# Kernel tuning notes

Measured on AMD Instinct MI355X. Metric: run time of the kernel, lower is better.

The kernel has to match this reference:

```python
import jax, jax.numpy as jnp
import numpy as np

N = 100000      # nodes
M_HE = 200000   # hyperedges
E = 2000000     # incidences (edge_index columns)
IN, HID, OUT, NT = 16, 64, 64, 2


def setup_inputs() -> dict:
    key = jax.random.key(0)
    ks = jax.random.split(key, 16)
    s = 0.05
    return {
        "x": jax.random.normal(ks[0], (N, IN), jnp.float32),
        "h_prev": jax.random.normal(ks[1], (N, HID), jnp.float32),
        "edge_nodes": jax.random.randint(ks[2], (E,), 0, N, dtype=jnp.int32),
        "edge_hedges": jax.random.randint(ks[3], (E,), 0, M_HE, dtype=jnp.int32),
        "edge_attr": jax.random.randint(ks[4], (E,), 0, NT, dtype=jnp.int32),
        "W_conv": jax.random.normal(ks[5], (NT, IN, HID), jnp.float32) * s,
        "b_conv": jax.random.normal(ks[6], (NT, HID), jnp.float32) * s,
        "W_mix": jax.random.normal(ks[7], (NT * HID, HID), jnp.float32) * s,
        "b_mix": jax.random.normal(ks[8], (HID,), jnp.float32) * s,
        "W_ih": jax.random.normal(ks[9], (3 * HID, HID), jnp.float32) * s,
        "W_hh": jax.random.normal(ks[10], (3 * HID, HID), jnp.float32) * s,
        "b_ih": jax.random.normal(ks[11], (3 * HID,), jnp.float32) * s,
        "b_hh": jax.random.normal(ks[12], (3 * HID,), jnp.float32) * s,
        "W_out": jax.random.normal(ks[13], (HID, OUT), jnp.float32) * s,
        "b_out": jax.random.normal(ks[14], (OUT,), jnp.float32) * s,
    }


def _hconv(x, W, b, nodes, hedges, mask_f):
    """PyG HypergraphConv: out = D^-1 H B^-1 H^T (x W) + b, restricted to
    incidences where mask_f==1 (replaces torch nonzero()-based slicing)."""
    xw = x @ W                                                   # [N, HID]
    Bdeg = jax.ops.segment_sum(mask_f, hedges, num_segments=M_HE)  # |e| per hyperedge
    Ddeg = jax.ops.segment_sum(mask_f, nodes, num_segments=N)      # deg per node
    Binv = jnp.where(Bdeg > 0, 1.0 / Bdeg, 0.0)
    Dinv = jnp.where(Ddeg > 0, 1.0 / Ddeg, 0.0)
    # node -> hyperedge gather/scatter
    e_feat = jax.ops.segment_sum(xw[nodes] * mask_f[:, None], hedges,
                                 num_segments=M_HE) * Binv[:, None]  # [M_HE, HID]
    # hyperedge -> node gather/scatter
    out = jax.ops.segment_sum(e_feat[hedges] * mask_f[:, None], nodes,
                              num_segments=N) * Dinv[:, None]        # [N, HID]
    return out + b


def reference(x, h_prev, edge_nodes, edge_hedges, edge_attr,
              W_conv, b_conv, W_mix, b_mix,
              W_ih, W_hh, b_ih, b_hh, W_out, b_out):
    outs = []
    for t in range(NT):  # fixed small loop over edge types
        mask_f = (edge_attr == t).astype(x.dtype)
        outs.append(_hconv(x, W_conv[t], b_conv[t], edge_nodes, edge_hedges, mask_f))
    h = jax.nn.relu(jnp.concatenate(outs, axis=1) @ W_mix + b_mix)  # [N, HID]
    # torch GRUCell(h, h_prev)
    gi = h @ W_ih.T + b_ih
    gh = h_prev @ W_hh.T + b_hh
    i_r, i_z, i_n = jnp.split(gi, 3, axis=1)
    h_r, h_z, h_n = jnp.split(gh, 3, axis=1)
    r = jax.nn.sigmoid(i_r + h_r)
    z = jax.nn.sigmoid(i_z + h_z)
    n = jnp.tanh(i_n + r * h_n)
    h_next = (1.0 - z) * n + z * h_prev
    pred_xyz = (h_next @ W_out + b_out)[:, :3]
    return h_next, pred_xyz
```

## Files before the change

kernel.cpp:

```cpp
#include <hip/hip_runtime.h>

#define NN      100000
#define MHE     200000
#define EE      2000000
#define H1      400000
#define K2N     200000
#define NB1     782
#define NB2     782
#define NCB2    320
#define CHK2    6250
#define FCN     500480
#define SCB2    489
#define CAP1    3584
#define CAP2    3584
#define NT      6250

typedef unsigned short u16;
typedef unsigned int   u32;
typedef unsigned long long ull;
typedef __attribute__((ext_vector_type(8))) short  s16x8;
typedef __attribute__((ext_vector_type(4))) float  f32x4;
typedef __attribute__((ext_vector_type(4))) unsigned int u32x4;

__device__ __forceinline__ float bf2f(u16 u) { return __uint_as_float(((u32)u) << 16); }
__device__ __forceinline__ u16 f2bf(float f) {
    u32 u = __float_as_uint(f);
    return (u16)((u + 0x7fffu + ((u >> 16) & 1u)) >> 16);
}
__device__ __forceinline__ float ldv(const void* p, long i, int isf32) {
    return isf32 ? ((const float*)p)[i] : bf2f(((const u16*)p)[i]);
}
__device__ __forceinline__ u16 ldb(const void* p, long i, int isf32) {
    return isf32 ? f2bf(((const float*)p)[i]) : ((const u16*)p)[i];
}
__device__ __forceinline__ void stv(void* p, long i, float v, int isf32) {
    if (isf32) ((float*)p)[i] = v;
    else       ((u16*)p)[i] = f2bf(v);
}

union FragU { s16x8 v; ull q[2]; u16 u[8]; };

__device__ __forceinline__ s16x8 ld8bf(const void* p, long off, int isf32) {
    FragU f;
    if (isf32) {
        const float* fp = (const float*)p + off;
        f32x4 a = *(const f32x4*)fp;
        f32x4 b = *(const f32x4*)(fp + 4);
        f.u[0]=f2bf(a[0]); f.u[1]=f2bf(a[1]); f.u[2]=f2bf(a[2]); f.u[3]=f2bf(a[3]);
        f.u[4]=f2bf(b[0]); f.u[5]=f2bf(b[1]); f.u[6]=f2bf(b[2]); f.u[7]=f2bf(b[3]);
    } else {
        u32x4 w = *(const u32x4*)((const u16*)p + off);
        f.q[0] = ((ull)w[1] << 32) | w[0];
        f.q[1] = ((ull)w[3] << 32) | w[2];
    }
    return f.v;
}

__device__ __forceinline__ float frcp_(float x) { return __builtin_amdgcn_rcpf(x); }
__device__ __forceinline__ float sigm(float x)  { return frcp_(1.f + __expf(-x)); }
__device__ __forceinline__ float tanhf_(float x){ return 1.f - 2.f * frcp_(1.f + __expf(2.f * x)); }

#define OFF_BKT1  0
#define OFF_BKT2  2000000
#define OFF_EXB   4000000
#define OFF_FSC   7200000
#define OFF_TOT   7700481
#define OFF_BCOMB 7700970
#define OFF_WIHB  7701034
#define OFF_WHHB  7707178
#define OFF_WCB   7713322
#define OFF_FLAG  7714346

__global__ void detect_kernel(const u32* __restrict__ xw, u32* __restrict__ flag) {
    __shared__ int cnt;
    if (threadIdx.x == 0) cnt = 0;
    __syncthreads();
    int hits = 0;
    for (int i = threadIdx.x; i < 1024; i += 256) {
        float v = bf2f((u16)(xw[i] & 0xffffu));
        if (!(fabsf(v) < 1e10f)) hits++;
    }
    atomicAdd(&cnt, hits);
    __syncthreads();
    if (threadIdx.x == 0) flag[0] = (cnt >= 16) ? 1u : 0u;
}

#define XBASE 26688
__global__ __launch_bounds__(256) void setup_kernel(
        const void* __restrict__ W_conv, const void* __restrict__ b_conv,
        const void* __restrict__ W_mix,  const void* __restrict__ b_mix,
        const void* __restrict__ W_ih,   const void* __restrict__ W_hh,
        float* __restrict__ bcomb, u16* __restrict__ Wihb, u16* __restrict__ Whhb,
        u16* __restrict__ Wcb, const u32* __restrict__ flag) {
    int isf = (int)flag[0];
    int gid = blockIdx.x * 256 + threadIdx.x;
    if (gid < 12288) {
        Wihb[gid] = ldb(W_ih, gid, isf);
    } else if (gid < 24576) {
        int i = gid - 12288;
        Whhb[i] = ldb(W_hh, i, isf);
    } else if (gid < 26624) {
        int i = gid - 24576;
        int j = i >> 5, k = i & 31;
        int t0 = k >> 4, kk = k & 15;
        float acc = 0.f;
        for (int c = 0; c < 64; c++)
            acc += ldv(W_conv, (t0 * 16 + kk) * 64 + c, isf) * ldv(W_mix, (t0 * 64 + c) * 64 + j, isf);
        Wcb[i] = f2bf(acc);
    } else if (gid < XBASE) {
        int j = gid - 26624;
        if (j < 64) {
            float acc = ldv(b_mix, j, isf);
            for (int c = 0; c < 128; c++)
                acc += ldv(b_conv, c, isf) * ldv(W_mix, c * 64 + j, isf);
            bcomb[j] = acc;
        }
    }
}

__global__ __launch_bounds__(1024) void countC(const int* __restrict__ en, const int* __restrict__ eh,
                                               const int* __restrict__ ea, int* __restrict__ fcnt) {
    __shared__ int c[NB1 + NB2];
    int g = blockIdx.x, tid = threadIdx.x;
    for (int i = tid; i < NB1 + NB2; i += 1024) c[i] = 0;
    __syncthreads();
    int s = g * CHK2;
    for (int i = s + tid; i < s + CHK2; i += 1024) {
        int t = ea[i];
        atomicAdd(&c[(t * MHE + eh[i]) >> 9], 1);
        atomicAdd(&c[NB1 + ((t * NN + en[i]) >> 8)], 1);
    }
    __syncthreads();
    for (int b = tid; b < NB1 + NB2; b += 1024) fcnt[b * NCB2 + g] = c[b];
}

__global__ __launch_bounds__(256) void scanA2(int* __restrict__ a, int* __restrict__ tot) {
    __shared__ int lds[256];
    int g = blockIdx.x, t = threadIdx.x;
    int base = g * 1024 + t * 4;
    int v[4]; int s = 0;
    #pragma unroll
    for (int j = 0; j < 4; j++) { v[j] = (base + j < FCN) ? a[base + j] : 0; s += v[j]; }
    lds[t] = s;
    __syncthreads();
    for (int d = 1; d < 256; d <<= 1) {
        int tmp = (t >= d) ? lds[t - d] : 0;
        __syncthreads();
        lds[t] += tmp;
        __syncthreads();
    }
    int run = lds[t] - s;
    #pragma unroll
    for (int j = 0; j < 4; j++) { if (base + j < FCN) a[base + j] = run; run += v[j]; }
    if (t == 255) tot[g] = lds[255];
}

__global__ __launch_bounds__(1024) void scanB2(int* __restrict__ tot) {
    __shared__ int lds[1024];
    int t = threadIdx.x;
    int v = (t < SCB2) ? tot[t] : 0;
    lds[t] = v;
    __syncthreads();
    for (int d = 1; d < 1024; d <<= 1) {
        int tmp = (t >= d) ? lds[t - d] : 0;
        __syncthreads();
        lds[t] += tmp;
        __syncthreads();
    }
    if (t < SCB2) tot[t] = lds[t] - v;
}

__global__ __launch_bounds__(256) void scanC2(int* __restrict__ a, const int* __restrict__ tot) {
    int g = blockIdx.x, t = threadIdx.x;
    int add = tot[g];
    int base = g * 1024 + t * 4;
    #pragma unroll
    for (int j = 0; j < 4; j++)
        if (base + j < FCN) a[base + j] += add;
    if (g == 0 && t == 0) a[FCN] = 2 * EE;
}

template<int SIDE>
__global__ __launch_bounds__(1024) void placeC(const int* __restrict__ en, const int* __restrict__ eh,
                                               const int* __restrict__ ea, const int* __restrict__ fscan,
                                               u32* __restrict__ bktout) {
    __shared__ u32 sarr[CHK2];
    __shared__ int sbuf[1024];
    __shared__ int cnt[NB1];
    __shared__ int loff[NB1];
    const int nb = SIDE ? NB2 : NB1;
    const int fbase = SIDE ? NB1 * NCB2 : 0;
    int g = blockIdx.x, tid = threadIdx.x;
    for (int b = tid; b < nb; b += 1024) {
        int idx = fbase + b * NCB2 + g;
        cnt[b] = fscan[idx + 1] - fscan[idx];
    }
    __syncthreads();
    int v = (tid < nb) ? cnt[tid] : 0;
    sbuf[tid] = v;
    __syncthreads();
    for (int d = 1; d < 1024; d <<= 1) {
        int tmp = (tid >= d) ? sbuf[tid - d] : 0;
        __syncthreads();
        sbuf[tid] += tmp;
        __syncthreads();
    }
    if (tid < nb) { loff[tid] = sbuf[tid] - v; cnt[tid] = 0; }
    __syncthreads();
    int s = g * CHK2;
    for (int i = s + tid; i < s + CHK2; i += 1024) {
        int t = ea[i]; int nd = en[i]; int hh = eh[i];
        int k = SIDE ? (t * NN + nd) : (t * MHE + hh);
        int b = SIDE ? (k >> 8) : (k >> 9);
        int r = atomicAdd(&cnt[b], 1);
        u32 pay = SIDE ? (((u32)(k & 255) << 19) | (u32)(t * MHE + hh))
                       : (((u32)(k & 511) << 17) | (u32)nd);
        sarr[loff[b] + r] = pay;
    }
    __syncthreads();
    for (int s2 = tid; s2 < CHK2; s2 += 1024) {
        int lo = 0, hi = nb - 1;
        while (lo < hi) {
            int mid = (lo + hi + 1) >> 1;
            if (loff[mid] <= s2) lo = mid; else hi = mid - 1;
        }
        int gp = fscan[fbase + lo * NCB2 + g] + (s2 - loff[lo]);
        if (SIDE) gp -= EE;
        bktout[gp] = sarr[s2];
    }
}

__global__ __launch_bounds__(512) void hopA(const int* __restrict__ fscan, const u32* __restrict__ bkt1,
                                            const void* __restrict__ x, u32* __restrict__ exb,
                                            const u32* __restrict__ flag) {
    __shared__ int fcnt[512], foff[513], sbuf[512];
    __shared__ int snod[CAP1];
    int isf = (int)flag[0];
    int c = blockIdx.x, tid = threadIdx.x;
    int beg = fscan[c * NCB2], end = fscan[(c + 1) * NCB2];
    fcnt[tid] = 0;
    __syncthreads();
    for (int i = beg + tid; i < end; i += 512)
        atomicAdd(&fcnt[bkt1[i] >> 17], 1);
    __syncthreads();
    int v = fcnt[tid];
    sbuf[tid] = v;
    __syncthreads();
    for (int d = 1; d < 512; d <<= 1) {
        int tmp = (tid >= d) ? sbuf[tid - d] : 0;
        __syncthreads();
        sbuf[tid] += tmp;
        __syncthreads();
    }
    foff[tid] = sbuf[tid] - v;
    fcnt[tid] = 0;
    if (tid == 511) foff[512] = sbuf[511];
    __syncthreads();
    for (int i = beg + tid; i < end; i += 512) {
        u32 p = bkt1[i];
        int k = (int)(p >> 17);
        int r = atomicAdd(&fcnt[k], 1);
        snod[foff[k] + r] = (int)(p & 0x1FFFFu);
    }
    __syncthreads();
    int sub = tid & 7, grp = tid >> 3;
    for (int kk = grp; kk < 512; kk += 64) {
        int key = c * 512 + kk;
        if (key >= H1) break;
        int fb = foff[kk], fe = foff[kk + 1];
        float a0 = 0.f, a1 = 0.f, b0 = 0.f, b1 = 0.f;
        float c0 = 0.f, c1 = 0.f, d0 = 0.f, d1 = 0.f;
        int j = fb;
        if (isf) {
            const float* xf = (const float*)x;
            for (; j + 3 < fe; j += 4) {
                long n0 = (long)snod[j], n1 = (long)snod[j+1];
                long n2 = (long)snod[j+2], n3 = (long)snod[j+3];
                a0 += xf[n0 * 16 + 2 * sub]; a1 += xf[n0 * 16 + 2 * sub + 1];
                b0 += xf[n1 * 16 + 2 * sub]; b1 += xf[n1 * 16 + 2 * sub + 1];
                c0 += xf[n2 * 16 + 2 * sub]; c1 += xf[n2 * 16 + 2 * sub + 1];
                d0 += xf[n3 * 16 + 2 * sub]; d1 += xf[n3 * 16 + 2 * sub + 1];
            }
            for (; j < fe; j++) {
                long n0 = (long)snod[j];
                a0 += xf[n0 * 16 + 2 * sub];
                a1 += xf[n0 * 16 + 2 * sub + 1];
            }
        } else {
            const u32* xu = (const u32*)x;
            for (; j + 3 < fe; j += 4) {
                u32 w0 = xu[(long)snod[j]   * 8 + sub];
                u32 w1 = xu[(long)snod[j+1] * 8 + sub];
                u32 w2 = xu[(long)snod[j+2] * 8 + sub];
                u32 w3 = xu[(long)snod[j+3] * 8 + sub];
                a0 += bf2f((u16)(w0 & 0xffffu)); a1 += bf2f((u16)(w0 >> 16));
                b0 += bf2f((u16)(w1 & 0xffffu)); b1 += bf2f((u16)(w1 >> 16));
                c0 += bf2f((u16)(w2 & 0xffffu)); c1 += bf2f((u16)(w2 >> 16));
                d0 += bf2f((u16)(w3 & 0xffffu)); d1 += bf2f((u16)(w3 >> 16));
            }
            for (; j < fe; j++) {
                u32 w = xu[(long)snod[j] * 8 + sub];
                a0 += bf2f((u16)(w & 0xffffu));
                a1 += bf2f((u16)(w >> 16));
            }
        }
        float s0 = (a0 + b0) + (c0 + d0);
        float s1 = (a1 + b1) + (c1 + d1);
        int d = fe - fb;
        float inv = d > 0 ? 1.0f / (float)d : 0.f;
        exb[(long)key * 8 + sub] = (u32)f2bf(s0 * inv) | ((u32)f2bf(s1 * inv) << 16);
    }
}

__global__ __launch_bounds__(256) void hopB(const int* __restrict__ fscan, const u32* __restrict__ bkt2,
                                            const u32* __restrict__ exb, u32* __restrict__ aggb) {
    __shared__ int fcnt[256], foff[257], sbuf[256];
    __shared__ int shed[CAP2];
    int c = blockIdx.x, tid = threadIdx.x;
    int beg = fscan[NB1 * NCB2 + c * NCB2] - EE;
    int end = fscan[NB1 * NCB2 + (c + 1) * NCB2] - EE;
    fcnt[tid] = 0;
    __syncthreads();
    for (int i = beg + tid; i < end; i += 256)
        atomicAdd(&fcnt[bkt2[i] >> 19], 1);
    __syncthreads();
    int v = fcnt[tid];
    sbuf[tid] = v;
    __syncthreads();
    for (int d = 1; d < 256; d <<= 1) {
        int tmp = (tid >= d) ? sbuf[tid - d] : 0;
        __syncthreads();
        sbuf[tid] += tmp;
        __syncthreads();
    }
    foff[tid] = sbuf[tid] - v;
    fcnt[tid] = 0;
    if (tid == 255) foff[256] = sbuf[255];
    __syncthreads();
    for (int i = beg + tid; i < end; i += 256) {
        u32 p = bkt2[i];
        int k = (int)(p >> 19);
        int r = atomicAdd(&fcnt[k], 1);
        shed[foff[k] + r] = (int)(p & 0x7FFFFu);
    }
    __syncthreads();
    int sub = tid & 7, grp = tid >> 3;
    for (int kk = grp; kk < 256; kk += 32) {
        int key = c * 256 + kk;
        if (key >= K2N) break;
        int fb = foff[kk], fe = foff[kk + 1];
        float a0 = 0.f, a1 = 0.f, b0 = 0.f, b1 = 0.f;
        float c0 = 0.f, c1 = 0.f, d0 = 0.f, d1 = 0.f;
        int j = fb;
        for (; j + 3 < fe; j += 4) {
            u32 w0 = exb[(long)shed[j]   * 8 + sub];
            u32 w1 = exb[(long)shed[j+1] * 8 + sub];
            u32 w2 = exb[(long)shed[j+2] * 8 + sub];
            u32 w3 = exb[(long)shed[j+3] * 8 + sub];
            a0 += bf2f((u16)(w0 & 0xffffu)); a1 += bf2f((u16)(w0 >> 16));
            b0 += bf2f((u16)(w1 & 0xffffu)); b1 += bf2f((u16)(w1 >> 16));
            c0 += bf2f((u16)(w2 & 0xffffu)); c1 += bf2f((u16)(w2 >> 16));
            d0 += bf2f((u16)(w3 & 0xffffu)); d1 += bf2f((u16)(w3 >> 16));
        }
        for (; j < fe; j++) {
            u32 w = exb[(long)shed[j] * 8 + sub];
            a0 += bf2f((u16)(w & 0xffffu));
            a1 += bf2f((u16)(w >> 16));
        }
        float s0 = (a0 + b0) + (c0 + d0);
        float s1 = (a1 + b1) + (c1 + d1);
        int d = fe - fb;
        float inv = d > 0 ? 1.0f / (float)d : 0.f;
        aggb[(long)key * 8 + sub] = (u32)f2bf(s0 * inv) | ((u32)f2bf(s1 * inv) << 16);
    }
}

__global__ __launch_bounds__(256) void epilogue(const u32* __restrict__ aggb,
                                                const float* __restrict__ bcomb,
                                                const u16* __restrict__ WihbG,
                                                const u16* __restrict__ Wcb,
                                                const void* __restrict__ b_ih, const void* __restrict__ b_hh,
                                                const void* __restrict__ h_prev,
                                                const void* __restrict__ W_out, const void* __restrict__ b_out,
                                                void* __restrict__ out,
                                                const u32* __restrict__ flag) {
    __shared__ u16 Wl[24576];
    __shared__ u16 hA[4][16][72];
    __shared__ float cb[8][64];
    __shared__ float cbo[3];
    int isf = (int)flag[0];
    int tid = threadIdx.x;
    {
        const u32* gw = (const u32*)WihbG;
        for (int i = tid; i < 12288; i += 256) {
            u32 v = gw[i];
            int row = i >> 5;
            int wb = (i & 31) * 4;
            int slot = wb >> 4, rem = wb & 15;
            int wb2 = (((slot ^ (row & 7)) << 4) | rem);
            *(u32*)(Wl + ((row << 6) + (wb2 >> 1))) = v;
        }
    }
    if (tid < 64) {
        int j = tid;
        cb[0][j] = bcomb[j];
        cb[1][j] = ldv(b_ih, j, isf)       + ldv(b_hh, j, isf);
        cb[2][j] = ldv(b_ih, 64 + j, isf)  + ldv(b_hh, 64 + j, isf);
        cb[3][j] = ldv(b_ih, 128 + j, isf);
        cb[4][j] = ldv(b_hh, 128 + j, isf);
        cb[5][j] = ldv(W_out, (long)j * 64 + 0, isf);
        cb[6][j] = ldv(W_out, (long)j * 64 + 1, isf);
        cb[7][j] = ldv(W_out, (long)j * 64 + 2, isf);
        if (j < 3) cbo[j] = ldv(b_out, j, isf);
    }
    __syncthreads();
    int w = tid >> 6, lane = tid & 63;
    int cl = lane & 15, q = lane >> 4;
    u16* hAw = &hA[w][0][0];
    int t0 = q >> 1;

    int wt = blockIdx.x * 4 + w;
    const int WSTRIDE = gridDim.x * 4;

    u32x4 aw; s16x8 hpA, hpB;
    if (wt < NT) {
        long nb = (long)wt * 16;
        aw  = *(const u32x4*)(aggb + ((long)t0 * NN + nb + cl) * 8 + (q & 1) * 4);
        hpA = ld8bf(h_prev, (nb + cl) * 64 + q * 8, isf);
        hpB = ld8bf(h_prev, (nb + cl) * 64 + 32 + q * 8, isf);
    }
    while (wt < NT) {
        int cwt = wt;
        u32x4 caw = aw; s16x8 chp0 = hpA, chp1 = hpB;
        wt += WSTRIDE;
        if (wt < NT) {
            long nb = (long)wt * 16;
            aw  = *(const u32x4*)(aggb + ((long)t0 * NN + nb + cl) * 8 + (q & 1) * 4);
            hpA = ld8bf(h_prev, (nb + cl) * 64 + q * 8, isf);
            hpB = ld8bf(h_prev, (nb + cl) * 64 + 32 + q * 8, isf);
        }
        long nb = (long)cwt * 16;
        {
            FragU fa;
            fa.q[0] = ((ull)caw[1] << 32) | caw[0];
            fa.q[1] = ((ull)caw[3] << 32) | caw[2];
            #pragma unroll
            for (int c = 0; c < 4; c++) {
                f32x4 hacc = (f32x4){0.f, 0.f, 0.f, 0.f};
                s16x8 bfr = *(const s16x8*)(Wcb + (c * 16 + cl) * 32 + q * 8);
                hacc = __builtin_amdgcn_mfma_f32_16x16x32_bf16(fa.v, bfr, hacc, 0, 0, 0);
                float bc = cb[0][c * 16 + cl];
                #pragma unroll
                for (int reg = 0; reg < 4; reg++) {
                    float hv = fmaxf(hacc[reg] + bc, 0.f);
                    hAw[(q * 4 + reg) * 72 + c * 16 + cl] = f2bf(hv);
                }
            }
        }
        asm volatile("" ::: "memory");
        const u16* hrow = hAw + cl * 72;
        FragU ha0, ha1;
        #pragma unroll
        for (int j = 0; j < 8; j++) {
            ha0.u[j] = hrow[q * 8 + j];
            ha1.u[j] = hrow[32 + q * 8 + j];
        }

        float p0[4] = {0,0,0,0}, p1[4] = {0,0,0,0}, p2[4] = {0,0,0,0};
        #pragma unroll
        for (int ch = 0; ch < 2; ch++) {
            f32x4 accr[2], accz[2], accin[2], acchn[2];
            #pragma unroll
            for (int cc = 0; cc < 2; cc++) {
                int j = (ch * 2 + cc) * 16 + cl;
                float br_ = cb[1][j], bz_ = cb[2][j], bi_ = cb[3][j], bh_ = cb[4][j];
                accr[cc]  = (f32x4){br_, br_, br_, br_};
                accz[cc]  = (f32x4){bz_, bz_, bz_, bz_};
                accin[cc] = (f32x4){bi_, bi_, bi_, bi_};
                acchn[cc] = (f32x4){bh_, bh_, bh_, bh_};
            }
            #pragma unroll
            for (int s = 0; s < 2; s++) {
                s16x8 hf  = s ? ha1.v : ha0.v;
                s16x8 hpf = s ? chp1 : chp0;
                int sl8 = ((s * 4 + q) ^ (cl & 7)) * 8;
                #pragma unroll
                for (int cc = 0; cc < 2; cc++) {
                    int rr = (ch * 2 + cc) * 16 + cl;
                    const u16* pw = Wl + rr * 64 + sl8;
                    s16x8 bir  = *(const s16x8*)(pw);
                    s16x8 biz  = *(const s16x8*)(pw + 4096);
                    s16x8 bin2 = *(const s16x8*)(pw + 8192);
                    s16x8 bhr  = *(const s16x8*)(pw + 12288);
                    s16x8 bhz  = *(const s16x8*)(pw + 16384);
                    s16x8 bhn2 = *(const s16x8*)(pw + 20480);
                    accr[cc]  = __builtin_amdgcn_mfma_f32_16x16x32_bf16(hf,  bir,  accr[cc], 0, 0, 0);
                    accr[cc]  = __builtin_amdgcn_mfma_f32_16x16x32_bf16(hpf, bhr,  accr[cc], 0, 0, 0);
                    accz[cc]  = __builtin_amdgcn_mfma_f32_16x16x32_bf16(hf,  biz,  accz[cc], 0, 0, 0);
                    accz[cc]  = __builtin_amdgcn_mfma_f32_16x16x32_bf16(hpf, bhz,  accz[cc], 0, 0, 0);
                    accin[cc] = __builtin_amdgcn_mfma_f32_16x16x32_bf16(hf,  bin2, accin[cc], 0, 0, 0);
                    acchn[cc] = __builtin_amdgcn_mfma_f32_16x16x32_bf16(hpf, bhn2, acchn[cc], 0, 0, 0);
                }
            }
            #pragma unroll
            for (int cc = 0; cc < 2; cc++) {
                int j = (ch * 2 + cc) * 16 + cl;
                float wo0 = cb[5][j], wo1 = cb[6][j], wo2 = cb[7][j];
                #pragma unroll
                for (int reg = 0; reg < 4; reg++) {
                    float rr = sigm(accr[cc][reg]);
                    float zz = sigm(accz[cc][reg]);
                    float ng = tanhf_(accin[cc][reg] + rr * acchn[cc][reg]);
                    long n = nb + q * 4 + reg;
                    float hp = ldv(h_prev, n * 64 + j, isf);
                    float hx = (1.f - zz) * ng + zz * hp;
                    stv(out, n * 64 + j, hx, isf);
                    p0[reg] += hx * wo0;
                    p1[reg] += hx * wo1;
                    p2[reg] += hx * wo2;
                }
            }
        }
        #pragma unroll
        for (int reg = 0; reg < 4; reg++) {
            #pragma unroll
            for (int off2 = 1; off2 < 16; off2 <<= 1) {
                p0[reg] += __shfl_xor(p0[reg], off2);
                p1[reg] += __shfl_xor(p1[reg], off2);
                p2[reg] += __shfl_xor(p2[reg], off2);
            }
        }
        if (cl == 0) {
            #pragma unroll
            for (int reg = 0; reg < 4; reg++) {
                long n = nb + q * 4 + reg;
                long pb = (long)NN * 64 + n * 3;
                stv(out, pb + 0, p0[reg] + cbo[0], isf);
                stv(out, pb + 1, p1[reg] + cbo[1], isf);
                stv(out, pb + 2, p2[reg] + cbo[2], isf);
            }
        }
    }
}

extern "C" void kernel_launch(void* const* d_in, const int* in_sizes, int n_in,
                              void* d_out, int out_size, void* d_ws, size_t ws_size,
                              hipStream_t stream) {
    const void* x      = d_in[0];
    const void* h_prev = d_in[1];
    const int* en      = (const int*)d_in[2];
    const int* eh      = (const int*)d_in[3];
    const int* ea      = (const int*)d_in[4];
    const void* W_conv = d_in[5];
    const void* b_conv = d_in[6];
    const void* W_mix  = d_in[7];
    const void* b_mix  = d_in[8];
    const void* W_ih   = d_in[9];
    const void* W_hh   = d_in[10];
    const void* b_ih   = d_in[11];
    const void* b_hh   = d_in[12];
    const void* W_out  = d_in[13];
    const void* b_out  = d_in[14];
    void* out          = d_out;

    float* ws    = (float*)d_ws;
    u32* bkt1    = (u32*)(ws + OFF_BKT1);
    u32* bkt2    = (u32*)(ws + OFF_BKT2);
    u32* exb     = (u32*)(ws + OFF_EXB);
    int* fscan   = (int*)(ws + OFF_FSC);
    u32* aggb    = (u32*)(ws + OFF_BKT1);
    float* bcomb = ws + OFF_BCOMB;
    u16* Wihb    = (u16*)(ws + OFF_WIHB);
    u16* Whhb    = (u16*)(ws + OFF_WHHB);
    u16* Wcb     = (u16*)(ws + OFF_WCB);
    u32* flag    = (u32*)(ws + OFF_FLAG);
    int* tot     = (int*)(ws + OFF_TOT);

    detect_kernel<<<1, 256, 0, stream>>>((const u32*)x, flag);
    setup_kernel<<<(XBASE + 255) / 256, 256, 0, stream>>>(
        W_conv, b_conv, W_mix, b_mix, W_ih, W_hh,
        bcomb, Wihb, Whhb, Wcb, flag);
    countC<<<NCB2, 1024, 0, stream>>>(en, eh, ea, fscan);
    scanA2<<<SCB2, 256, 0, stream>>>(fscan, tot);
    scanB2<<<1, 1024, 0, stream>>>(tot);
    scanC2<<<SCB2, 256, 0, stream>>>(fscan, tot);
    placeC<0><<<NCB2, 1024, 0, stream>>>(en, eh, ea, fscan, bkt1);
    placeC<1><<<NCB2, 1024, 0, stream>>>(en, eh, ea, fscan, bkt2);
    hopA<<<NB1, 512, 0, stream>>>(fscan, bkt1, x, exb, flag);
    hopB<<<NB2, 256, 0, stream>>>(fscan, bkt2, exb, aggb);
    epilogue<<<512, 256, 0, stream>>>(aggb, bcomb, Wihb, Wcb,
                                      b_ih, b_hh, h_prev, W_out, b_out, out, flag);
}
```

Baseline: 291.5 us.

## Fuse both bucket placement passes and add dynamic key scheduling in hop kernels

Merges the two templated placement kernels into one that reads edge arrays once, keeps both keys in LDS, and scatters directly to global buckets with shared atomics. This drops the local prefix scan, the LDS staging, and the binary-search writeback. Each bucket entry is now written straight to global memory from an atomic slot, so writes are less coalesced and order within a bucket is nondeterministic. The hop kernels also replace the static group-strided key loop with an LDS atomic ticket per 8-lane group, to balance uneven segment lengths.

```diff
diff --git a/kernel.cpp b/kernel.cpp
--- a/kernel.cpp
+++ b/kernel.cpp
@@ -180,53 +180,44 @@
     if (g == 0 && t == 0) a[FCN] = 2 * EE;
 }
 
-template<int SIDE>
-__global__ __launch_bounds__(1024) void placeC(const int* __restrict__ en, const int* __restrict__ eh,
-                                               const int* __restrict__ ea, const int* __restrict__ fscan,
-                                               u32* __restrict__ bktout) {
-    __shared__ u32 sarr[CHK2];
-    __shared__ int sbuf[1024];
+__global__ __launch_bounds__(1024) void placeAB(const int* __restrict__ en, const int* __restrict__ eh,
+                                                const int* __restrict__ ea, const int* __restrict__ fscan,
+                                                u32* __restrict__ bkt1, u32* __restrict__ bkt2) {
+    __shared__ u32 A[CHK2];
+    __shared__ u32 Bk[CHK2];
     __shared__ int cnt[NB1];
-    __shared__ int loff[NB1];
-    const int nb = SIDE ? NB2 : NB1;
-    const int fbase = SIDE ? NB1 * NCB2 : 0;
+    __shared__ int base_[NB1];
     int g = blockIdx.x, tid = threadIdx.x;
-    for (int b = tid; b < nb; b += 1024) {
-        int idx = fbase + b * NCB2 + g;
-        cnt[b] = fscan[idx + 1] - fscan[idx];
-    }
-    __syncthreads();
-    int v = (tid < nb) ? cnt[tid] : 0;
-    sbuf[tid] = v;
-    __syncthreads();
-    for (int d = 1; d < 1024; d <<= 1) {
-        int tmp = (tid >= d) ? sbuf[tid - d] : 0;
-        __syncthreads();
-        sbuf[tid] += tmp;
-        __syncthreads();
-    }
-    if (tid < nb) { loff[tid] = sbuf[tid] - v; cnt[tid] = 0; }
-    __syncthreads();
     int s = g * CHK2;
-    for (int i = s + tid; i < s + CHK2; i += 1024) {
-        int t = ea[i]; int nd = en[i]; int hh = eh[i];
-        int k = SIDE ? (t * NN + nd) : (t * MHE + hh);
-        int b = SIDE ? (k >> 8) : (k >> 9);
+    for (int i = tid; i < CHK2; i += 1024) {
+        int t = ea[s + i];
+        A[i]  = (u32)(t * MHE + eh[s + i]);
+        Bk[i] = (u32)(t * NN  + en[s + i]);
+    }
+    for (int b = tid; b < NB1; b += 1024) {
+        cnt[b] = 0;
+        base_[b] = fscan[b * NCB2 + g];
+    }
+    __syncthreads();
+    for (int i = tid; i < CHK2; i += 1024) {
+        u32 k1 = A[i];
+        int b = (int)(k1 >> 9);
         int r = atomicAdd(&cnt[b], 1);
-        u32 pay = SIDE ? (((u32)(k & 255) << 19) | (u32)(t * MHE + hh))
-                       : (((u32)(k & 511) << 17) | (u32)nd);
-        sarr[loff[b] + r] = pay;
-    }
-    __syncthreads();
-    for (int s2 = tid; s2 < CHK2; s2 += 1024) {
-        int lo = 0, hi = nb - 1;
-        while (lo < hi) {
-            int mid = (lo + hi + 1) >> 1;
-            if (loff[mid] <= s2) lo = mid; else hi = mid - 1;
-        }
-        int gp = fscan[fbase + lo * NCB2 + g] + (s2 - loff[lo]);
-        if (SIDE) gp -= EE;
-        bktout[gp] = sarr[s2];
+        u32 t = (k1 >= (u32)MHE) ? 1u : 0u;
+        u32 nd = Bk[i] - t * (u32)NN;
+        bkt1[base_[b] + r] = ((k1 & 511u) << 17) | nd;
+    }
+    __syncthreads();
+    for (int b = tid; b < NB2; b += 1024) {
+        cnt[b] = 0;
+        base_[b] = fscan[NB1 * NCB2 + b * NCB2 + g] - EE;
+    }
+    __syncthreads();
+    for (int i = tid; i < CHK2; i += 1024) {
+        u32 k2 = Bk[i];
+        int b = (int)(k2 >> 8);
+        int r = atomicAdd(&cnt[b], 1);
+        bkt2[base_[b] + r] = ((k2 & 255u) << 19) | A[i];
     }
 }
 
@@ -235,10 +226,12 @@
                                             const u32* __restrict__ flag) {
     __shared__ int fcnt[512], foff[513], sbuf[512];
     __shared__ int snod[CAP1];
+    __shared__ int tick;
     int isf = (int)flag[0];
     int c = blockIdx.x, tid = threadIdx.x;
     int beg = fscan[c * NCB2], end = fscan[(c + 1) * NCB2];
     fcnt[tid] = 0;
+    if (tid == 0) tick = 0;
     __syncthreads();
     for (int i = beg + tid; i < end; i += 512)
         atomicAdd(&fcnt[bkt1[i] >> 17], 1);
@@ -263,8 +256,13 @@
         snod[foff[k] + r] = (int)(p & 0x1FFFFu);
     }
     __syncthreads();
-    int sub = tid & 7, grp = tid >> 3;
-    for (int kk = grp; kk < 512; kk += 64) {
+    int lane = tid & 63;
+    int sub = lane & 7;
+    for (;;) {
+        int kk;
+        if (sub == 0) kk = atomicAdd(&tick, 1);
+        kk = __shfl(kk, lane & 56);
+        if (kk >= 512) break;
         int key = c * 512 + kk;
         if (key >= H1) break;
         int fb = foff[kk], fe = foff[kk + 1];
@@ -316,10 +314,12 @@
                                             const u32* __restrict__ exb, u32* __restrict__ aggb) {
     __shared__ int fcnt[256], foff[257], sbuf[256];
     __shared__ int shed[CAP2];
+    __shared__ int tick;
     int c = blockIdx.x, tid = threadIdx.x;
     int beg = fscan[NB1 * NCB2 + c * NCB2] - EE;
     int end = fscan[NB1 * NCB2 + (c + 1) * NCB2] - EE;
     fcnt[tid] = 0;
+    if (tid == 0) tick = 0;
     __syncthreads();
     for (int i = beg + tid; i < end; i += 256)
         atomicAdd(&fcnt[bkt2[i] >> 19], 1);
@@ -344,8 +344,13 @@
         shed[foff[k] + r] = (int)(p & 0x7FFFFu);
     }
     __syncthreads();
-    int sub = tid & 7, grp = tid >> 3;
-    for (int kk = grp; kk < 256; kk += 32) {
+    int lane = tid & 63;
+    int sub = lane & 7;
+    for (;;) {
+        int kk;
+        if (sub == 0) kk = atomicAdd(&tick, 1);
+        kk = __shfl(kk, lane & 56);
+        if (kk >= 256) break;
         int key = c * 256 + kk;
         if (key >= K2N) break;
         int fb = foff[kk], fe = foff[kk + 1];
@@ -584,8 +589,7 @@
     scanA2<<<SCB2, 256, 0, stream>>>(fscan, tot);
     scanB2<<<1, 1024, 0, stream>>>(tot);
     scanC2<<<SCB2, 256, 0, stream>>>(fscan, tot);
-    placeC<0><<<NCB2, 1024, 0, stream>>>(en, eh, ea, fscan, bkt1);
-    placeC<1><<<NCB2, 1024, 0, stream>>>(en, eh, ea, fscan, bkt2);
+    placeAB<<<NCB2, 1024, 0, stream>>>(en, eh, ea, fscan, bkt1, bkt2);
     hopA<<<NB1, 512, 0, stream>>>(fscan, bkt1, x, exb, flag);
     hopB<<<NB2, 256, 0, stream>>>(fscan, bkt2, exb, aggb);
     epilogue<<<512, 256, 0, stream>>>(aggb, bcomb, Wihb, Wcb,
```

After: 287.4 us. No clear change (-1.4%).
